# Optimization experiments

Measured on AMD Instinct MI355X. Metric: run time of the kernel, lower is better.

The kernel has to match this reference:

```python
import jax, jax.numpy as jnp
import numpy as np

HEADS = 12

def setup_inputs() -> dict:
    key = jax.random.key(0)
    k1, k2, k3 = jax.random.split(key, 3)
    b, n, d = 8, 1024, 768
    x = jax.random.normal(k1, (b, n, d), dtype=jnp.float32)
    # xavier_uniform-like init for linear weights
    lim_qkv = float(np.sqrt(6.0 / (d + 3 * d)))
    W_qkv = jax.random.uniform(k2, (3 * d, d), dtype=jnp.float32, minval=-lim_qkv, maxval=lim_qkv)
    b_qkv = jnp.zeros((3 * d,), dtype=jnp.float32)
    lim_o = float(np.sqrt(6.0 / (d + d)))
    W_out = jax.random.uniform(k3, (d, d), dtype=jnp.float32, minval=-lim_o, maxval=lim_o)
    b_out = jnp.zeros((d,), dtype=jnp.float32)
    return {"x": x, "W_qkv": W_qkv, "b_qkv": b_qkv, "W_out": W_out, "b_out": b_out}

def reference(x, W_qkv, b_qkv, W_out, b_out):
    b, n, d = x.shape
    h = HEADS
    hd = d // h
    scale = d ** (-0.5)  # NOTE: original scales by dim**-0.5, not head_dim**-0.5
    qkv = x @ W_qkv.T + b_qkv                      # [b, n, 3d]
    q, k, v = jnp.split(qkv, 3, axis=-1)           # each [b, n, d]
    def to_heads(t):
        return t.reshape(b, n, h, hd).transpose(0, 2, 1, 3)  # [b, h, n, hd]
    q, k, v = to_heads(q), to_heads(k), to_heads(v)
    dots = jnp.einsum('bhid,bhjd->bhij', q, k) * scale       # [b, h, n, n]
    attn = jax.nn.softmax(dots, axis=-1)
    out = jnp.einsum('bhij,bhjd->bhid', attn, v)             # [b, h, n, hd]
    out = out.transpose(0, 2, 1, 3).reshape(b, n, d)
    return out @ W_out.T + b_out
```

## Files before the change

kernel.cpp:

```cpp
#include <hip/hip_runtime.h>
#include <stdint.h>

typedef __bf16 bf16x8 __attribute__((ext_vector_type(8)));
typedef float  f32x4  __attribute__((ext_vector_type(4)));
typedef unsigned short u16;

#define AS1 __attribute__((address_space(1)))
#define AS3 __attribute__((address_space(3)))
#define G2L(gp, lp) __builtin_amdgcn_global_load_lds( \
    (const AS1 unsigned int*)(uintptr_t)(gp), \
    (AS3 unsigned int*)(uintptr_t)(lp), 16, 0, 0)

static __device__ __forceinline__ u16 f32_to_bf16(float f) {
    unsigned u = __float_as_uint(f);
    u += 0x7fffu + ((u >> 16) & 1u);
    return (u16)(u >> 16);
}

static __device__ __forceinline__ unsigned pack_bf16(float lo, float hi) {
    return (unsigned)f32_to_bf16(lo) | ((unsigned)f32_to_bf16(hi) << 16);
}

static __device__ __forceinline__ float fast_exp2(float x) {
    return __builtin_amdgcn_exp2f(x);
}

static __device__ __forceinline__ f32x4 mfma16(bf16x8 a, bf16x8 b, f32x4 c) {
    return __builtin_amdgcn_mfma_f32_16x16x32_bf16(a, b, c, 0, 0, 0);
}

__global__ void cvt3_k(const float* __restrict__ a, const float* __restrict__ b,
                       const float* __restrict__ c, u16* __restrict__ out) {
    const int i = blockIdx.x * blockDim.x + threadIdx.x;
    const float* src; int off;
    if (i < 1572864)      { src = a; off = 0; }
    else if (i < 2015232) { src = b; off = 1572864; }
    else                  { src = c; off = 2015232; }
    const float4 v = reinterpret_cast<const float4*>(src)[i - off];
    reinterpret_cast<uint2*>(out)[i] = make_uint2(pack_bf16(v.x, v.y), pack_bf16(v.z, v.w));
}

template<int OUTF32>
__global__ __launch_bounds__(256, 3) void gemm_bt_k(const u16* __restrict__ A, const u16* __restrict__ B,
                                                    const float* __restrict__ bias, void* __restrict__ Cp,
                                                    int M, int N, int K) {
    __shared__ __align__(16) u16 As[128 * 64];
    __shared__ __align__(16) u16 Bs[128 * 64];
    const int t = threadIdx.x, w = t >> 6, l = t & 63, lr = l & 15, lg = l >> 4;
    const int wr = w >> 1, wc = w & 1;
    const long rowBase = (long)blockIdx.y * 128;
    const long colBase = (long)blockIdx.x * 128;

    const f32x4 z = {0.f, 0.f, 0.f, 0.f};
    f32x4 acc[4][4];
    #pragma unroll
    for (int m = 0; m < 4; ++m)
        #pragma unroll
        for (int n = 0; n < 4; ++n) acc[m][n] = z;

    const int kSteps = K >> 6;
    for (int kt = 0; kt < kSteps; ++kt) {
        const int k0 = kt << 6;
        __syncthreads();
        #pragma unroll
        for (int i = 0; i < 4; ++i) {
            const int c = i * 256 + t;
            const int row = c >> 3, ch = c & 7;
            const int sch = ch ^ (row & 7);
            G2L(A + (rowBase + row) * K + k0 + sch * 8, As + (i * 256 + w * 64) * 8);
            G2L(B + (colBase + row) * K + k0 + sch * 8, Bs + (i * 256 + w * 64) * 8);
        }
        __syncthreads();
        #pragma unroll
        for (int kk = 0; kk < 2; ++kk) {
            bf16x8 af[4], bfr[4];
            #pragma unroll
            for (int m = 0; m < 4; ++m) {
                const int row = wr * 64 + m * 16 + lr;
                af[m] = *reinterpret_cast<const bf16x8*>(&As[row * 64 + (((kk * 4 + lg) ^ (lr & 7)) << 3)]);
            }
            #pragma unroll
            for (int n = 0; n < 4; ++n) {
                const int row = wc * 64 + n * 16 + lr;
                bfr[n] = *reinterpret_cast<const bf16x8*>(&Bs[row * 64 + (((kk * 4 + lg) ^ (lr & 7)) << 3)]);
            }
            #pragma unroll
            for (int m = 0; m < 4; ++m)
                #pragma unroll
                for (int n = 0; n < 4; ++n) acc[m][n] = mfma16(af[m], bfr[n], acc[m][n]);
        }
    }
    #pragma unroll
    for (int n = 0; n < 4; ++n) {
        const long gc = colBase + wc * 64 + n * 16 + lr;
        const float bv = bias[gc];
        #pragma unroll
        for (int m = 0; m < 4; ++m) {
            const long gr = rowBase + wr * 64 + m * 16 + lg * 4;
            #pragma unroll
            for (int r = 0; r < 4; ++r) {
                const float v = acc[m][n][r] + bv;
                if (OUTF32) reinterpret_cast<float*>(Cp)[(gr + r) * N + gc] = v;
                else        reinterpret_cast<u16*>(Cp)[(gr + r) * N + gc] = f32_to_bf16(v);
            }
        }
    }
}

__global__ __launch_bounds__(256) void transpose_v_k(const u16* __restrict__ qkv, u16* __restrict__ vt) {
    const int bh = blockIdx.y, b = bh / 12, h = bh % 12;
    const int nt = blockIdx.x;
    __shared__ __align__(16) u16 Ts[64][72];
    const int t = threadIdx.x;
    const int rr = t >> 2;
    #pragma unroll
    for (int i = 0; i < 2; ++i) {
        const int ch = (t & 3) + i * 4;
        const u16* src = qkv + (long)(b * 1024 + nt * 64 + rr) * 2304 + 1536 + h * 64 + ch * 8;
        *reinterpret_cast<uint4*>(&Ts[rr][ch * 8]) = *reinterpret_cast<const uint4*>(src);
    }
    __syncthreads();
    #pragma unroll
    for (int i = 0; i < 2; ++i) {
        const int ch = (t & 3) + i * 4;
        u16 vals[8];
        #pragma unroll
        for (int j = 0; j < 8; ++j)
            vals[j] = Ts[(j & 3) * 16 + ch * 2 + (j >> 2)][rr];
        u16* dst = vt + (long)(bh * 64 + rr) * 1024 + nt * 64 + ch * 8;
        *reinterpret_cast<uint4*>(dst) = *reinterpret_cast<const uint4*>(vals);
    }
}

__global__ __launch_bounds__(256, 2) void attn_k(const u16* __restrict__ qkv, const u16* __restrict__ vt,
                                                 u16* __restrict__ outp) {
    const int id = blockIdx.x;
    const int bh = id % 96, qt = id / 96;
    const int b = bh / 12, h = bh % 12;
    const int t = threadIdx.x, w = t >> 6, l = t & 63, lr = l & 15, lg = l >> 4;
    __shared__ __align__(16) u16 Ks[2][64 * 64];
    __shared__ __align__(16) u16 Vts[2][64 * 64];
    __shared__ __align__(16) u16 Ps[4 * 16 * 64];

    const u16* kb = qkv + 768 + h * 64;
    const u16* vb = vt + (long)bh * 64 * 1024;

    #pragma unroll
    for (int i = 0; i < 2; ++i) {
        const int c = (i * 4 + w) * 64 + l;
        const int row = c >> 3, sch = (c & 7) ^ (row & 7);
        G2L(kb + (long)(b * 1024 + row) * 2304 + sch * 8, &Ks[0][(i * 4 + w) * 512]);
        G2L(vb + (long)row * 1024 + sch * 8, &Vts[0][(i * 4 + w) * 512]);
    }
    #pragma unroll
    for (int j = 0; j < 2; ++j) {
        const int c = j * 256 + t, row = c >> 3, ch = c & 7;
        const uint4 q = *reinterpret_cast<const uint4*>(
            qkv + (long)(b * 1024 + qt * 64 + row) * 2304 + h * 64 + ch * 8);
        *reinterpret_cast<uint4*>(&Ps[row * 64 + ((ch ^ (row & 7)) << 3)]) = q;
    }
    __syncthreads();
    bf16x8 aq[2];
    #pragma unroll
    for (int kk = 0; kk < 2; ++kk)
        aq[kk] = *reinterpret_cast<const bf16x8*>(&Ps[(w * 16 + lr) * 64 + (((kk * 4 + lg) ^ (lr & 7)) << 3)]);

    const f32x4 z = {0.f, 0.f, 0.f, 0.f};
    f32x4 o[4] = {z, z, z, z};
    float lacc[4] = {0.f, 0.f, 0.f, 0.f};
    const float sc2 = 0.052058773f;

    for (int kt = 0; kt < 16; ++kt) {
        const int cur = kt & 1;
        asm volatile("s_waitcnt vmcnt(0)" ::: "memory");
        __builtin_amdgcn_sched_barrier(0);
        __builtin_amdgcn_s_barrier();
        __builtin_amdgcn_sched_barrier(0);
        if (kt < 15) {
            const int ktn = kt + 1;
            #pragma unroll
            for (int i = 0; i < 2; ++i) {
                const int c = (i * 4 + w) * 64 + l;
                const int row = c >> 3, sch = (c & 7) ^ (row & 7);
                G2L(kb + (long)(b * 1024 + ktn * 64 + row) * 2304 + sch * 8, &Ks[cur ^ 1][(i * 4 + w) * 512]);
                G2L(vb + (long)row * 1024 + ktn * 64 + sch * 8, &Vts[cur ^ 1][(i * 4 + w) * 512]);
            }
        }
        __builtin_amdgcn_sched_barrier(0);
        f32x4 s[4] = {z, z, z, z};
        #pragma unroll
        for (int kk = 0; kk < 2; ++kk) {
            #pragma unroll
            for (int kc = 0; kc < 4; ++kc) {
                const int row = kc * 16 + lr;
                bf16x8 bk = *reinterpret_cast<const bf16x8*>(&Ks[cur][row * 64 + (((kk * 4 + lg) ^ (lr & 7)) << 3)]);
                s[kc] = mfma16(aq[kk], bk, s[kc]);
            }
        }
        #pragma unroll
        for (int r = 0; r < 4; ++r) {
            const float p0 = fast_exp2(s[0][r] * sc2);
            const float p1 = fast_exp2(s[1][r] * sc2);
            const float p2 = fast_exp2(s[2][r] * sc2);
            const float p3 = fast_exp2(s[3][r] * sc2);
            lacc[r] += (p0 + p1) + (p2 + p3);
            const unsigned w0 = pack_bf16(p0, p1);
            const unsigned w1 = pack_bf16(p2, p3);
            const int q = lg * 4 + r;
            const int csw = (lr >> 1) ^ (q & 7);
            *reinterpret_cast<uint2*>(&Ps[w * 1024 + q * 64 + csw * 8 + (lr & 1) * 4]) = make_uint2(w0, w1);
        }
        #pragma unroll
        for (int kk = 0; kk < 2; ++kk) {
            bf16x8 pa = *reinterpret_cast<const bf16x8*>(&Ps[w * 1024 + lr * 64 + (((kk * 4 + lg) ^ (lr & 7)) << 3)]);
            #pragma unroll
            for (int n = 0; n < 4; ++n) {
                const int row = n * 16 + lr;
                bf16x8 vbf = *reinterpret_cast<const bf16x8*>(&Vts[cur][row * 64 + (((kk * 4 + lg) ^ (lr & 7)) << 3)]);
                o[n] = mfma16(pa, vbf, o[n]);
            }
        }
    }
    #pragma unroll
    for (int r = 0; r < 4; ++r) {
        float rs = lacc[r];
        #pragma unroll
        for (int off = 1; off < 16; off <<= 1) rs += __shfl_xor(rs, off, 64);
        lacc[r] = rs;
    }
    const int qrow = qt * 64 + w * 16 + lg * 4;
    #pragma unroll
    for (int n = 0; n < 4; ++n) {
        #pragma unroll
        for (int r = 0; r < 4; ++r) {
            const float v = o[n][r] / lacc[r];
            outp[(long)(b * 1024 + qrow + r) * 768 + h * 64 + n * 16 + lr] = f32_to_bf16(v);
        }
    }
}

extern "C" void kernel_launch(void* const* d_in, const int* in_sizes, int n_in,
                              void* d_out, int out_size, void* d_ws, size_t ws_size,
                              hipStream_t stream) {
    (void)in_sizes; (void)n_in; (void)out_size; (void)ws_size;
    const float* x    = (const float*)d_in[0];
    const float* Wqkv = (const float*)d_in[1];
    const float* bqkv = (const float*)d_in[2];
    const float* Wout = (const float*)d_in[3];
    const float* bout = (const float*)d_in[4];

    u16* xb   = (u16*)d_ws;
    u16* Wqb  = xb  + 6291456;
    u16* Wob  = Wqb + 1769472;
    u16* qkv  = Wob + 589824;
    u16* vtb  = qkv + 18874368;
    u16* attn = vtb + 6291456;

    cvt3_k<<<8448, 256, 0, stream>>>(x, Wqkv, Wout, xb);

    gemm_bt_k<0><<<dim3(18, 64), 256, 0, stream>>>(xb, Wqb, bqkv, qkv, 8192, 2304, 768);
    transpose_v_k<<<dim3(16, 96), 256, 0, stream>>>(qkv, vtb);
    attn_k<<<1536, 256, 0, stream>>>(qkv, vtb, attn);
    gemm_bt_k<1><<<dim3(6, 64), 256, 0, stream>>>(attn, Wob, bout, d_out, 8192, 768, 768);
}
```

Measured before the change: 121.7 us.

## Double-buffer GEMM LDS tiles, swizzle block order, raise attention occupancy

The GEMM kernel now uses two LDS buffers and issues global-to-LDS loads for the next K tile before computing on the current one, with a single barrier per step instead of two. This is meant to hide global memory latency behind MFMA work. The grid is flattened to 1D and remapped with an XCD-aware swizzle (id&7) to improve L2 locality across chiplets. GEMM launch bounds drop to 2 blocks per CU because LDS use doubles, and the attention kernel's launch bound is raised to 4, which may force register spilling.

```diff
diff --git a/kernel.cpp b/kernel.cpp
--- a/kernel.cpp
+++ b/kernel.cpp
@@ -41,15 +41,19 @@
 }
 
 template<int OUTF32>
-__global__ __launch_bounds__(256, 3) void gemm_bt_k(const u16* __restrict__ A, const u16* __restrict__ B,
+__global__ __launch_bounds__(256, 2) void gemm_bt_k(const u16* __restrict__ A, const u16* __restrict__ B,
                                                     const float* __restrict__ bias, void* __restrict__ Cp,
-                                                    int M, int N, int K) {
-    __shared__ __align__(16) u16 As[128 * 64];
-    __shared__ __align__(16) u16 Bs[128 * 64];
+                                                    int M, int N, int K, int nbx) {
+    __shared__ __align__(16) u16 As[2][128 * 64];
+    __shared__ __align__(16) u16 Bs[2][128 * 64];
+    const int id = blockIdx.x;
+    const int cpx = gridDim.x >> 3;
+    const int swz = (id & 7) * cpx + (id >> 3);
+    const int bx = swz % nbx, by = swz / nbx;
     const int t = threadIdx.x, w = t >> 6, l = t & 63, lr = l & 15, lg = l >> 4;
     const int wr = w >> 1, wc = w & 1;
-    const long rowBase = (long)blockIdx.y * 128;
-    const long colBase = (long)blockIdx.x * 128;
+    const long rowBase = (long)by * 128;
+    const long colBase = (long)bx * 128;
 
     const f32x4 z = {0.f, 0.f, 0.f, 0.f};
     f32x4 acc[4][4];
@@ -59,30 +63,42 @@
         for (int n = 0; n < 4; ++n) acc[m][n] = z;
 
     const int kSteps = K >> 6;
+    #pragma unroll
+    for (int i = 0; i < 4; ++i) {
+        const int c = i * 256 + t, row = c >> 3, ch = c & 7;
+        const int sch = ch ^ (row & 7);
+        G2L(A + (rowBase + row) * K + sch * 8, &As[0][(i * 256 + w * 64) * 8]);
+        G2L(B + (colBase + row) * K + sch * 8, &Bs[0][(i * 256 + w * 64) * 8]);
+    }
     for (int kt = 0; kt < kSteps; ++kt) {
-        const int k0 = kt << 6;
-        __syncthreads();
-        #pragma unroll
-        for (int i = 0; i < 4; ++i) {
-            const int c = i * 256 + t;
-            const int row = c >> 3, ch = c & 7;
-            const int sch = ch ^ (row & 7);
-            G2L(A + (rowBase + row) * K + k0 + sch * 8, As + (i * 256 + w * 64) * 8);
-            G2L(B + (colBase + row) * K + k0 + sch * 8, Bs + (i * 256 + w * 64) * 8);
-        }
-        __syncthreads();
+        const int cur = kt & 1;
+        asm volatile("s_waitcnt vmcnt(0)" ::: "memory");
+        __builtin_amdgcn_sched_barrier(0);
+        __builtin_amdgcn_s_barrier();
+        __builtin_amdgcn_sched_barrier(0);
+        if (kt + 1 < kSteps) {
+            const int k0 = (kt + 1) << 6;
+            #pragma unroll
+            for (int i = 0; i < 4; ++i) {
+                const int c = i * 256 + t, row = c >> 3, ch = c & 7;
+                const int sch = ch ^ (row & 7);
+                G2L(A + (rowBase + row) * K + k0 + sch * 8, &As[cur ^ 1][(i * 256 + w * 64) * 8]);
+                G2L(B + (colBase + row) * K + k0 + sch * 8, &Bs[cur ^ 1][(i * 256 + w * 64) * 8]);
+            }
+        }
+        __builtin_amdgcn_sched_barrier(0);
         #pragma unroll
         for (int kk = 0; kk < 2; ++kk) {
             bf16x8 af[4], bfr[4];
             #pragma unroll
             for (int m = 0; m < 4; ++m) {
                 const int row = wr * 64 + m * 16 + lr;
-                af[m] = *reinterpret_cast<const bf16x8*>(&As[row * 64 + (((kk * 4 + lg) ^ (lr & 7)) << 3)]);
+                af[m] = *reinterpret_cast<const bf16x8*>(&As[cur][row * 64 + (((kk * 4 + lg) ^ (lr & 7)) << 3)]);
             }
             #pragma unroll
             for (int n = 0; n < 4; ++n) {
                 const int row = wc * 64 + n * 16 + lr;
-                bfr[n] = *reinterpret_cast<const bf16x8*>(&Bs[row * 64 + (((kk * 4 + lg) ^ (lr & 7)) << 3)]);
+                bfr[n] = *reinterpret_cast<const bf16x8*>(&Bs[cur][row * 64 + (((kk * 4 + lg) ^ (lr & 7)) << 3)]);
             }
             #pragma unroll
             for (int m = 0; m < 4; ++m)
@@ -132,7 +148,7 @@
     }
 }
 
-__global__ __launch_bounds__(256, 2) void attn_k(const u16* __restrict__ qkv, const u16* __restrict__ vt,
+__global__ __launch_bounds__(256, 4) void attn_k(const u16* __restrict__ qkv, const u16* __restrict__ vt,
                                                  u16* __restrict__ outp) {
     const int id = blockIdx.x;
     const int bh = id % 96, qt = id / 96;
@@ -258,8 +274,8 @@
 
     cvt3_k<<<8448, 256, 0, stream>>>(x, Wqkv, Wout, xb);
 
-    gemm_bt_k<0><<<dim3(18, 64), 256, 0, stream>>>(xb, Wqb, bqkv, qkv, 8192, 2304, 768);
+    gemm_bt_k<0><<<1152, 256, 0, stream>>>(xb, Wqb, bqkv, qkv, 8192, 2304, 768, 18);
     transpose_v_k<<<dim3(16, 96), 256, 0, stream>>>(qkv, vtb);
     attn_k<<<1536, 256, 0, stream>>>(qkv, vtb, attn);
-    gemm_bt_k<1><<<dim3(6, 64), 256, 0, stream>>>(attn, Wob, bout, d_out, 8192, 768, 768);
-}
+    gemm_bt_k<1><<<384, 256, 0, stream>>>(attn, Wob, bout, d_out, 8192, 768, 768, 6);
+}
```

Measured after the change: 116.1 us. 4.6% less time.
